# Optimization experiments

Measured on AMD Instinct MI355X. Metric: run time of the kernel, lower is better.

The kernel has to match this reference:

```python
import jax, jax.numpy as jnp
import numpy as np

B, N, D, CI, CO = 16, 1024, 16, 128, 128
ITERS = 3
EPS_BN = 1e-5
EPS_SQ = 1e-8


def sparsemax(z, axis):
    # Martins & Astudillo sparsemax along `axis`.
    K = z.shape[axis]
    z_s = jnp.flip(jnp.sort(z, axis=axis), axis=axis)  # descending
    z_cum = jnp.cumsum(z_s, axis=axis)
    shp = [1] * z.ndim
    shp[axis] = K
    k = jnp.arange(1, K + 1, dtype=z.dtype).reshape(shp)
    support = 1.0 + k * z_s > z_cum
    k_z = jnp.sum(support, axis=axis, keepdims=True).astype(z.dtype)
    tau_sum = jnp.sum(jnp.where(support, z_s, 0.0), axis=axis, keepdims=True)
    tau = (tau_sum - 1.0) / k_z
    return jnp.maximum(z - tau, 0.0)


def squash(s, axis):
    sq = jnp.sum(s * s, axis=axis, keepdims=True)
    return (sq / (1.0 + sq)) * s / jnp.sqrt(sq + EPS_SQ)


def setup_inputs() -> dict:
    key = jax.random.key(0)
    ks = jax.random.split(key, 4)
    x = jax.random.normal(ks[0], (B, N, CI), jnp.float32)
    a = jax.random.uniform(ks[1], (B, N, N), jnp.float32)
    adj = (a < 0.02).astype(jnp.float32)
    adj = jnp.maximum(adj, jnp.swapaxes(adj, -1, -2))  # symmetric 0/1 adjacency
    bn_gamma = jnp.ones((CI,), jnp.float32)
    bn_beta = jnp.zeros((CI,), jnp.float32)
    W = jax.random.normal(ks[2], (D, CI, CO), jnp.float32) / np.sqrt(CI)
    bias = jnp.zeros((D, CO), jnp.float32)
    return {"x": x, "adj": adj, "bn_gamma": bn_gamma, "bn_beta": bn_beta,
            "W": W, "bias": bias}


def _forward(x, adj, bn_gamma, bn_beta, W, bias):
    # BatchNorm1d, training-mode batch stats over flattened [B*N, CI]
    xf = x.reshape(-1, x.shape[-1])
    mu = xf.mean(0)
    var = ((xf - mu) ** 2).mean(0)  # biased variance (torch BN normalization)
    xn = (x - mu) / jnp.sqrt(var + EPS_BN) * bn_gamma + bn_beta

    # DenseGCNConv per digit capsule; adjacency normalization is shared.
    n = adj.shape[-1]
    eye = jnp.eye(n, dtype=adj.dtype)
    a = adj * (1.0 - eye) + eye                    # diag set to 1 (self-loops)
    dis = jnp.clip(a.sum(-1), 1.0, None) ** -0.5
    a_norm = dis[:, :, None] * a * dis[:, None, :]  # D^-1/2 A D^-1/2
    xw = jnp.einsum('bni,dio->bndo', xn, W)
    u = jnp.einsum('bmn,bndo->bmdo', a_norm, xw) + bias  # u_hat [B,N,D,CO]

    u_det = jax.lax.stop_gradient(u)  # torch uses u_hat.detach() in the loop
    b = jnp.zeros(u.shape[:3], u.dtype)  # [B,N,D]
    for _ in range(ITERS - 1):
        c = sparsemax(b, axis=2)
        s = jnp.einsum('bnd,bndo->bdo', c, u_det)
        v = squash(s, axis=-1)  # squash over capsule dim (dim=-2 in torch view)
        b = b + jnp.einsum('bndo,bdo->bnd', u_det, v)

    c = sparsemax(b, axis=2)
    s = jnp.einsum('bnd,bndo->bdo', c, u)
    s = s + xn.mean(1)[:, None, :]  # residual; broadcasts over D (needs CI==CO)
    # Original squashes with dim=-1 over a trailing singleton -> elementwise squash
    sq = s * s
    v = (sq / (1.0 + sq)) * s / jnp.sqrt(sq + EPS_SQ)

    adj_out = jnp.einsum('bnd,bnm,bme->bde', c, adj, c)  # coarsened adjacency
    return v, adj_out


def reference(x, adj, bn_gamma, bn_beta, W, bias):
    return _forward(x, adj, bn_gamma, bn_beta, W, bias)
```

## Files before the change

kernel.cpp:

```cpp
#include <hip/hip_runtime.h>

#define NB 16
#define NN 1024
#define ND 16
#define NCI 128
#define NCO 128
#define BN_ROWS (NB*NN)
#define MAXDEG 128
#define VOFF_ADJ (NB*ND*NCO)

__device__ __forceinline__ void fma4(float4& a, float s, const float4& w) {
    a.x = fmaf(s, w.x, a.x); a.y = fmaf(s, w.y, a.y);
    a.z = fmaf(s, w.z, a.z); a.w = fmaf(s, w.w, a.w);
}
__device__ __forceinline__ void add4(float4& a, const float4& b) {
    a.x += b.x; a.y += b.y; a.z += b.z; a.w += b.w;
}

__global__ __launch_bounds__(256) void k_pre1(const float* __restrict__ x,
                                              float* __restrict__ pbn,
                                              const float* __restrict__ W,
                                              float* __restrict__ Wt) {
    __shared__ float4 ls[8][32], lq[8][32];
    __shared__ float tile[32][33];
    int t = threadIdx.x;
    if (blockIdx.x < 256) {
        int q = t & 31, rg = t >> 5;
        int row0 = blockIdx.x * 64;
        const float4* x4 = (const float4*)x;
        float4 s = make_float4(0, 0, 0, 0), sq = make_float4(0, 0, 0, 0);
        for (int r = rg; r < 64; r += 8) {
            float4 v = x4[(size_t)(row0 + r) * 32 + q];
            s.x += v.x; s.y += v.y; s.z += v.z; s.w += v.w;
            sq.x = fmaf(v.x, v.x, sq.x); sq.y = fmaf(v.y, v.y, sq.y);
            sq.z = fmaf(v.z, v.z, sq.z); sq.w = fmaf(v.w, v.w, sq.w);
        }
        ls[rg][q] = s; lq[rg][q] = sq;
        __syncthreads();
        if (t < 32) {
            float4 a = ls[0][t];
            #pragma unroll
            for (int r = 1; r < 8; ++r) add4(a, ls[r][t]);
            ((float4*)(pbn + (size_t)blockIdx.x * 256))[t] = a;
        } else if (t < 64) {
            int qq = t - 32;
            float4 a = lq[0][qq];
            #pragma unroll
            for (int r = 1; r < 8; ++r) add4(a, lq[r][qq]);
            ((float4*)(pbn + (size_t)blockIdx.x * 256 + 128))[qq] = a;
        }
    } else {
        int d = blockIdx.x - 256;
        int r = t >> 5, cq = t & 31;
        const float* Wd = W + (size_t)d * NCI * NCO;
        float* Wtd = Wt + (size_t)d * NCI * NCO;
        for (int ti = 0; ti < 4; ++ti)
            for (int tj = 0; tj < 4; ++tj) {
                __syncthreads();
                for (int rr = r; rr < 32; rr += 8)
                    tile[rr][cq] = Wd[(size_t)(ti * 32 + rr) * 128 + tj * 32 + cq];
                __syncthreads();
                for (int rr = r; rr < 32; rr += 8)
                    Wtd[(size_t)(tj * 32 + rr) * 128 + ti * 32 + cq] = tile[cq][rr];
            }
    }
}

__global__ __launch_bounds__(256) void k_pre2(const float* __restrict__ adj,
        float* __restrict__ dis, int* __restrict__ nbr_idx, int* __restrict__ nbr_cnt,
        float* __restrict__ selfd, const float* __restrict__ pbn,
        const float* __restrict__ gamma, const float* __restrict__ beta,
        float* __restrict__ ss, float* __restrict__ xm) {
    int t = threadIdx.x;
    if (blockIdx.x < NB * NN) {
        int bm = blockIdx.x;
        int m = bm & (NN - 1);
        const float4* row4 = (const float4*)(adj + (size_t)bm * NN);
        __shared__ int cnt;
        __shared__ int idx[MAXDEG];
        if (t == 0) { cnt = 1; idx[0] = m; }
        __syncthreads();
        float4 v = row4[t];
        int n0 = t * 4;
        float av[4] = {v.x, v.y, v.z, v.w};
        #pragma unroll
        for (int j = 0; j < 4; ++j) {
            int n = n0 + j;
            if (n == m) {
                selfd[bm] = (av[j] > 0.5f) ? 1.f : 0.f;
            } else if (av[j] > 0.5f) {
                int p = atomicAdd(&cnt, 1);
                if (p < MAXDEG) idx[p] = n;
            }
        }
        __syncthreads();
        int c = min(cnt, MAXDEG);
        if (t == 0) {
            nbr_cnt[bm] = c;
            dis[bm] = rsqrtf((float)c);
        }
        for (int k = t; k < c; k += 256) nbr_idx[(size_t)bm * MAXDEG + k] = idx[k];
    } else {
        int b = blockIdx.x - NB * NN;
        if (t < 128) {
            float s = 0.f, sq = 0.f, sb = 0.f;
            for (int blk = 0; blk < 256; ++blk) {
                float v = pbn[(size_t)blk * 256 + t];
                s += v;
                sq += pbn[(size_t)blk * 256 + 128 + t];
                sb += ((blk >> 4) == b) ? v : 0.f;
            }
            float mu = s * (1.f / BN_ROWS);
            float var = sq * (1.f / BN_ROWS) - mu * mu;
            float sc = gamma[t] * rsqrtf(var + 1e-5f);
            float sh = beta[t] - mu * sc;
            if (b == 0) { ss[t] = sc; ss[128 + t] = sh; }
            xm[b * NCI + t] = sb * (1.f / NN) * sc + sh;
        }
    }
}

__global__ void k_y(const float* __restrict__ x, const float* __restrict__ ss,
                    const float* __restrict__ dis, const int* __restrict__ nbr_idx,
                    const int* __restrict__ nbr_cnt, float* __restrict__ y) {
    int l = blockIdx.x;
    int idx0 = l >> 3;
    int b = (l & 7) + ((idx0 >> 10) << 3);
    int m = idx0 & 1023;
    int bm = (b << 10) + m;
    int t = threadIdx.x;
    int q = t & 31, ng = t >> 5;
    __shared__ float sw[MAXDEG];
    __shared__ int sIdx[MAXDEG];
    int cnt = nbr_cnt[bm];
    float dm = dis[bm];
    for (int k = t; k < cnt; k += 128) {
        int n = nbr_idx[(size_t)bm * MAXDEG + k];
        sIdx[k] = n;
        sw[k] = dm * dis[(b << 10) + n];
    }
    __syncthreads();
    const float4* xb = (const float4*)(x + ((size_t)(b << 10)) * NCI);
    float4 acc = make_float4(0, 0, 0, 0);
    float wsum = 0.f;
    for (int k = ng; k < cnt; k += 4) {
        float w = sw[k];
        float4 v = xb[(size_t)sIdx[k] * 32 + q];
        fma4(acc, w, v);
        wsum += w;
    }
    __shared__ float4 lacc[4][32];
    __shared__ float lws[4];
    lacc[ng][q] = acc;
    if (q == 0) lws[ng] = wsum;
    __syncthreads();
    if (t < 32) {
        float4 a = lacc[0][t];
        add4(a, lacc[1][t]); add4(a, lacc[2][t]); add4(a, lacc[3][t]);
        float wst = lws[0] + lws[1] + lws[2] + lws[3];
        float4 sc = ((const float4*)ss)[t];
        float4 sh = ((const float4*)(ss + 128))[t];
        float4 o;
        o.x = sc.x * a.x + sh.x * wst;
        o.y = sc.y * a.y + sh.y * wst;
        o.z = sc.z * a.z + sh.z * wst;
        o.w = sc.w * a.w + sh.w * wst;
        ((float4*)(y + (size_t)bm * NCI))[t] = o;
    }
}

__device__ __forceinline__ void sv_phase(int b, int d, int t, int mode,
    const float* __restrict__ gsrc, const float* __restrict__ pcs,
    const float* __restrict__ W, const float* __restrict__ Wt,
    const float* __restrict__ bias, const float* __restrict__ xm,
    float* __restrict__ hbuf, float* __restrict__ hbb, float* __restrict__ outv,
    float* gl, float4 (*red)[32], float* redf, float* svec, float* vvv,
    float* csum_s, float* scal)
{
    if (mode == 0) {
        int q = t & 31, rg = t >> 5;
        const float4* yb = (const float4*)(gsrc + (((size_t)b) << 10) * NCI);
        float4 s = make_float4(0, 0, 0, 0);
        #pragma unroll 4
        for (int r = rg; r < 1024; r += 8) add4(s, yb[(size_t)r * 32 + q]);
        red[rg][q] = s;
        if (t == 0) *csum_s = 64.f;
        __syncthreads();
        if (t < 32) {
            float4 a = red[0][t];
            #pragma unroll
            for (int r = 1; r < 8; ++r) add4(a, red[r][t]);
            a.x *= (1.f / 16.f); a.y *= (1.f / 16.f);
            a.z *= (1.f / 16.f); a.w *= (1.f / 16.f);
            ((float4*)gl)[t] = a;
        }
        __syncthreads();
    } else {
        int col = t & 127, half = t >> 7;
        float g = 0.f;
        #pragma unroll 4
        for (int ch = half * 16; ch < half * 16 + 16; ++ch)
            g += gsrc[(((size_t)b * 32 + ch) * 16 + d) * NCI + col];
        ((float*)red)[half * 128 + col] = g;
        if (t == 0) {
            float cs = 0.f;
            #pragma unroll
            for (int ch = 0; ch < 32; ++ch) cs += pcs[(b * 32 + ch) * 16 + d];
            *csum_s = cs;
        }
        __syncthreads();
        if (t < 128) gl[t] = ((float*)red)[t] + ((float*)red)[128 + t];
        __syncthreads();
    }

    {
        int q = t & 31, hh = t >> 5;
        const float4* Wd4 = (const float4*)(W + (size_t)d * NCI * NCO);
        float4 acc = make_float4(0, 0, 0, 0);
        for (int i = hh * 16; i < hh * 16 + 16; ++i)
            fma4(acc, gl[i], Wd4[(size_t)i * 32 + q]);
        red[hh][q] = acc;
    }
    __syncthreads();
    if (t < 32) {
        float4 a = red[0][t];
        #pragma unroll
        for (int r = 1; r < 8; ++r) add4(a, red[r][t]);
        float4 b4 = ((const float4*)(bias + d * NCO))[t];
        float cs = *csum_s;
        a.x = fmaf(cs, b4.x, a.x); a.y = fmaf(cs, b4.y, a.y);
        a.z = fmaf(cs, b4.z, a.z); a.w = fmaf(cs, b4.w, a.w);
        ((float4*)svec)[t] = a;
    }
    __syncthreads();

    if (mode == 2) {
        if (t < 128) {
            float sv2 = svec[t] + xm[b * NCO + t];
            float sq = sv2 * sv2;
            outv[(size_t)(b * 16 + d) * NCO + t] = (sq / (1.f + sq)) * sv2 * rsqrtf(sq + 1e-8f);
        }
        return;
    }

    redf[t] = (t < 128) ? svec[t] * svec[t] : 0.f;
    __syncthreads();
    if (t < 64) {
        float val = redf[t] + redf[t + 64] + redf[t + 128] + redf[t + 192];
        #pragma unroll
        for (int m2 = 32; m2 >= 1; m2 >>= 1) val += __shfl_xor(val, m2);
        if (t == 0) *scal = val;
    }
    __syncthreads();
    if (t < 128) {
        float tot = *scal;
        vvv[t] = (tot / (1.f + tot)) * svec[t] * rsqrtf(tot + 1e-8f);
    }
    __syncthreads();

    {
        int q = t & 31, hh = t >> 5;
        const float4* Wt4 = (const float4*)(Wt + (size_t)d * NCI * NCO);
        float4 acc = make_float4(0, 0, 0, 0);
        for (int o = hh * 16; o < hh * 16 + 16; ++o)
            fma4(acc, vvv[o], Wt4[(size_t)o * 32 + q]);
        red[hh][q] = acc;
    }
    redf[t] = (t < 128) ? bias[d * NCO + t] * vvv[t] : 0.f;
    __syncthreads();
    if (t < 32) {
        float4 a = red[0][t];
        #pragma unroll
        for (int r = 1; r < 8; ++r) add4(a, red[r][t]);
        ((float4*)(hbuf + (size_t)(b * 16 + d) * NCI))[t] = a;
    }
    if (t >= 64 && t < 128) {
        int tt = t - 64;
        float val = redf[tt] + redf[tt + 64] + redf[tt + 128] + redf[tt + 192];
        #pragma unroll
        for (int m2 = 32; m2 >= 1; m2 >>= 1) val += __shfl_xor(val, m2);
        if (tt == 0) hbb[b * 16 + d] = val;
    }
}

__global__ __launch_bounds__(256) void k_sv(const float* __restrict__ gsrc,
        const float* __restrict__ pcs, const float* __restrict__ W,
        const float* __restrict__ Wt, const float* __restrict__ bias,
        const float* __restrict__ xm, float* __restrict__ hbuf,
        float* __restrict__ hbb, float* __restrict__ outv, int mode) {
    __shared__ float gl[128], svec[128], vvv[128];
    __shared__ float4 red[8][32];
    __shared__ float redf[256];
    __shared__ float csum_s, scal;
    int l = blockIdx.x, idx0 = l >> 3;
    int b = (l & 7) + ((idx0 >> 4) << 3);
    int d = idx0 & 15;
    sv_phase(b, d, threadIdx.x, mode, gsrc, pcs, W, Wt, bias, xm,
             hbuf, hbb, outv, gl, red, redf, svec, vvv, &csum_s, &scal);
}

__global__ __launch_bounds__(256) void k_bgc(const float* __restrict__ y,
        const float* __restrict__ hbuf, const float* __restrict__ hbb,
        float* __restrict__ blog, float* __restrict__ cglob,
        float* __restrict__ pg, float* __restrict__ pcs,
        float* __restrict__ outz, int first, int last) {
    int l = blockIdx.x, idx0 = l >> 3;
    int b = (l & 7) + ((idx0 >> 5) << 3);
    int j = idx0 & 31;
    int t = threadIdx.x;
    int n0 = j * 32;
    __shared__ __align__(16) float sy[32 * 128];
    __shared__ __align__(16) float sh[16 * 132];
    __shared__ float shb[16];
    __shared__ float scd[32][17];
    {
        const float4* hb4 = (const float4*)(hbuf + (size_t)b * 16 * NCI);
        float4* sh4 = (float4*)sh;
        for (int jj = t; jj < 16 * 32; jj += 256) {
            int row = jj >> 5, col = jj & 31;
            sh4[row * 33 + col] = hb4[row * 32 + col];
        }
        const float4* yb4 = (const float4*)(y + (((size_t)b << 10) + n0) * NCI);
        float4* sy4 = (float4*)sy;
        for (int jj = t; jj < 32 * 32; jj += 256) sy4[jj] = yb4[jj];
        if (t < 16) shb[t] = hbb[b * 16 + t];
    }
    __syncthreads();
    int nsub = t >> 4, d = t & 15;
    #pragma unroll
    for (int nn = nsub; nn < 32; nn += 16) {
        float acc = 0.f;
        const float* yr = &sy[nn * 128];
        const float* hr = &sh[d * 132];
        #pragma unroll 8
        for (int i = 0; i < 128; i += 4) {
            float4 a = *(const float4*)&yr[i];
            float4 h4 = *(const float4*)&hr[i];
            acc = fmaf(a.x, h4.x, acc);
            acc = fmaf(a.y, h4.y, acc);
            acc = fmaf(a.z, h4.z, acc);
            acc = fmaf(a.w, h4.w, acc);
        }
        size_t idx = (((size_t)b << 10) + n0 + nn) * ND + d;
        float bnew = acc + shb[d] + (first ? 0.f : blog[idx]);
        if (!last) blog[idx] = bnew;
        scd[nn][d] = bnew;
    }
    __syncthreads();
    if (t < 32) {
        float z[16], zs[16];
        #pragma unroll
        for (int d2 = 0; d2 < 16; ++d2) { z[d2] = scd[t][d2]; zs[d2] = z[d2]; }
        #pragma unroll
        for (int a = 0; a < 16; ++a) {
            #pragma unroll
            for (int b2 = a + 1; b2 < 16; ++b2) {
                float hi = fmaxf(zs[a], zs[b2]);
                float lo = fminf(zs[a], zs[b2]);
                zs[a] = hi; zs[b2] = lo;
            }
        }
        float cs = 0.f, tausum = 0.f;
        int kz = 1;
        #pragma unroll
        for (int k = 1; k <= 16; ++k) {
            cs += zs[k - 1];
            if (1.f + (float)k * zs[k - 1] > cs) { kz = k; tausum = cs; }
        }
        float tau = (tausum - 1.f) / (float)kz;
        #pragma unroll
        for (int d2 = 0; d2 < 16; ++d2) scd[t][d2] = fmaxf(z[d2] - tau, 0.f);
    }
    __syncthreads();
    if (last) {
        for (int jj = t; jj < 32 * 16; jj += 256)
            cglob[(((size_t)b << 10) + n0 + (jj >> 4)) * ND + (jj & 15)] = scd[jj >> 4][jj & 15];
        if (j == 0) outz[VOFF_ADJ + b * 256 + t] = 0.f;
    }
    if (t < 16) {
        float cs = 0.f;
        #pragma unroll 4
        for (int nn = 0; nn < 32; ++nn) cs += scd[nn][t];
        pcs[(b * 32 + j) * 16 + t] = cs;
    }
    int col = t & 127, dh = t >> 7;
    float accg[8] = {};
    for (int nn = 0; nn < 32; ++nn) {
        float yv = sy[nn * 128 + col];
        #pragma unroll
        for (int dd = 0; dd < 8; ++dd) accg[dd] = fmaf(scd[nn][dh * 8 + dd], yv, accg[dd]);
    }
    #pragma unroll
    for (int dd = 0; dd < 8; ++dd)
        pg[(((size_t)b * 32 + j) * 16 + dh * 8 + dd) * NCI + col] = accg[dd];
}

__global__ __launch_bounds__(256) void k_svt(const float* __restrict__ pg,
        const float* __restrict__ pcs, const float* __restrict__ W,
        const float* __restrict__ Wt, const float* __restrict__ bias,
        const float* __restrict__ xm, float* __restrict__ hbuf,
        float* __restrict__ hbb, const float* __restrict__ cglob,
        const int* __restrict__ nbr_idx, const int* __restrict__ nbr_cnt,
        const float* __restrict__ selfd, float* __restrict__ outv) {
    __shared__ float gl[128], svec[128], vvv[128];
    __shared__ float4 red[8][32];
    __shared__ float redf[256];
    __shared__ float csum_s, scal;
    __shared__ float cm[32][17], tm[32][17];
    int t = threadIdx.x;
    if (blockIdx.x < 256) {
        int l = blockIdx.x, idx0 = l >> 3;
        int b = (l & 7) + ((idx0 >> 4) << 3);
        int d = idx0 & 15;
        sv_phase(b, d, t, 2, pg, pcs, W, Wt, bias, xm,
                 hbuf, hbb, outv, gl, red, redf, svec, vvv, &csum_s, &scal);
        return;
    }
    int l2 = blockIdx.x - 256, idx0 = l2 >> 3;
    int b = (l2 & 7) + ((idx0 >> 5) << 3);
    int j = idx0 & 31;
    for (int jj = t; jj < 32 * 16; jj += 256)
        cm[jj >> 4][jj & 15] = cglob[(((size_t)b << 10) + j * 32 + (jj >> 4)) * ND + (jj & 15)];
    __syncthreads();
    int w = t >> 6, tg = t & 63, nsub = tg >> 4, d = tg & 15;
    for (int mm = w; mm < 32; mm += 4) {
        int m = j * 32 + mm;
        int bm = (b << 10) + m;
        int cnt = nbr_cnt[bm];
        float acc = 0.f;
        for (int k = nsub; k < cnt; k += 4) {
            int n = nbr_idx[(size_t)bm * MAXDEG + k];
            acc += cglob[(((size_t)b << 10) + n) * ND + d];
        }
        acc += __shfl_xor(acc, 16);
        acc += __shfl_xor(acc, 32);
        if (tg < 16) {
            if (selfd[bm] == 0.f) acc -= cm[mm][d];
            tm[mm][d] = acc;
        }
    }
    __syncthreads();
    int d2 = t >> 4, e2 = t & 15;
    float s = 0.f;
    #pragma unroll 8
    for (int mm = 0; mm < 32; ++mm) s = fmaf(tm[mm][d2], cm[mm][e2], s);
    atomicAdd(&outv[VOFF_ADJ + b * 256 + t], s);
}

extern "C" void kernel_launch(void* const* d_in, const int* in_sizes, int n_in,
                              void* d_out, int out_size, void* d_ws, size_t ws_size,
                              hipStream_t stream) {
    const float* x     = (const float*)d_in[0];
    const float* adj   = (const float*)d_in[1];
    const float* gamma = (const float*)d_in[2];
    const float* beta  = (const float*)d_in[3];
    const float* W     = (const float*)d_in[4];
    const float* bias  = (const float*)d_in[5];
    float* out = (float*)d_out;

    char* wptr = (char*)d_ws;
    size_t used = 0;
    auto alloc = [&](size_t nbytes) -> void* {
        void* p = wptr + used;
        used += (nbytes + 255) & ~(size_t)255;
        return p;
    };
    float* pbn     = (float*)alloc((size_t)256 * 256 * 4);
    float* ss      = (float*)alloc(256 * 4);
    float* xm      = (float*)alloc((size_t)NB * NCI * 4);
    float* dis     = (float*)alloc((size_t)NB * NN * 4);
    float* selfd   = (float*)alloc((size_t)NB * NN * 4);
    int*   nbr_cnt = (int*)alloc((size_t)NB * NN * 4);
    float* Wt      = (float*)alloc((size_t)ND * NCI * NCO * 4);
    float* y       = (float*)alloc((size_t)NB * NN * NCI * 4);
    float* blog    = (float*)alloc((size_t)NB * NN * ND * 4);
    float* cglob   = (float*)alloc((size_t)NB * NN * ND * 4);
    float* pg      = (float*)alloc((size_t)NB * 32 * ND * NCI * 4);
    float* pcs     = (float*)alloc((size_t)NB * 32 * ND * 4);
    float* hbuf    = (float*)alloc((size_t)NB * ND * NCI * 4);
    float* hbb     = (float*)alloc((size_t)NB * ND * 4);
    int*   nbr_idx = (int*)alloc((size_t)NB * NN * MAXDEG * 4);
    if (used > ws_size) return;

    k_pre1<<<256 + ND, 256, 0, stream>>>(x, pbn, W, Wt);
    k_pre2<<<NB * NN + NB, 256, 0, stream>>>(adj, dis, nbr_idx, nbr_cnt, selfd,
                                             pbn, gamma, beta, ss, xm);
    k_y<<<NB * NN, 128, 0, stream>>>(x, ss, dis, nbr_idx, nbr_cnt, y);

    k_sv<<<NB * ND, 256, 0, stream>>>(y, pcs, W, Wt, bias, xm, hbuf, hbb, out, 0);
    k_bgc<<<NB * 32, 256, 0, stream>>>(y, hbuf, hbb, blog, cglob, pg, pcs, out, 1, 0);
    k_sv<<<NB * ND, 256, 0, stream>>>(pg, pcs, W, Wt, bias, xm, hbuf, hbb, out, 1);
    k_bgc<<<NB * 32, 256, 0, stream>>>(y, hbuf, hbb, blog, cglob, pg, pcs, out, 0, 1);
    k_svt<<<256 + NB * 32, 256, 0, stream>>>(pg, pcs, W, Wt, bias, xm, hbuf, hbb,
                                             cglob, nbr_idx, nbr_cnt, selfd, out);
}
```

Measured before the change: 138.2 us.

## Fuse sv and bgc routing kernels with per-batch atomic flag handoff

```diff
diff --git a/kernel.cpp b/kernel.cpp
--- a/kernel.cpp
+++ b/kernel.cpp
@@ -122,13 +122,15 @@
 
 __global__ void k_y(const float* __restrict__ x, const float* __restrict__ ss,
                     const float* __restrict__ dis, const int* __restrict__ nbr_idx,
-                    const int* __restrict__ nbr_cnt, float* __restrict__ y) {
+                    const int* __restrict__ nbr_cnt, float* __restrict__ y,
+                    int* __restrict__ done) {
     int l = blockIdx.x;
     int idx0 = l >> 3;
     int b = (l & 7) + ((idx0 >> 10) << 3);
     int m = idx0 & 1023;
     int bm = (b << 10) + m;
     int t = threadIdx.x;
+    if (l == 0 && t < 32) done[t] = 0;
     int q = t & 31, ng = t >> 5;
     __shared__ float sw[MAXDEG];
     __shared__ int sIdx[MAXDEG];
@@ -283,36 +285,61 @@
     }
 }
 
-__global__ __launch_bounds__(256) void k_sv(const float* __restrict__ gsrc,
-        const float* __restrict__ pcs, const float* __restrict__ W,
-        const float* __restrict__ Wt, const float* __restrict__ bias,
-        const float* __restrict__ xm, float* __restrict__ hbuf,
-        float* __restrict__ hbb, float* __restrict__ outv, int mode) {
-    __shared__ float gl[128], svec[128], vvv[128];
-    __shared__ float4 red[8][32];
-    __shared__ float redf[256];
-    __shared__ float csum_s, scal;
-    int l = blockIdx.x, idx0 = l >> 3;
-    int b = (l & 7) + ((idx0 >> 4) << 3);
-    int d = idx0 & 15;
-    sv_phase(b, d, threadIdx.x, mode, gsrc, pcs, W, Wt, bias, xm,
-             hbuf, hbb, outv, gl, red, redf, svec, vvv, &csum_s, &scal);
-}
-
-__global__ __launch_bounds__(256) void k_bgc(const float* __restrict__ y,
-        const float* __restrict__ hbuf, const float* __restrict__ hbb,
+__global__ __launch_bounds__(256) void k_f(const float* __restrict__ y,
+        const float* __restrict__ W, const float* __restrict__ Wt,
+        const float* __restrict__ bias, const float* __restrict__ xm,
+        float* __restrict__ hbuf, float* __restrict__ hbb,
         float* __restrict__ blog, float* __restrict__ cglob,
         float* __restrict__ pg, float* __restrict__ pcs,
-        float* __restrict__ outz, int first, int last) {
-    int l = blockIdx.x, idx0 = l >> 3;
-    int b = (l & 7) + ((idx0 >> 5) << 3);
+        float* __restrict__ outv, int* __restrict__ done, int iter) {
+    __shared__ __align__(16) char smem[27136];
+    int t = threadIdx.x;
+    int* flag = done + (iter == 2 ? 16 : 0);
+
+    if (blockIdx.x < 256) {
+        float* gl   = (float*)(smem);
+        float* svec = (float*)(smem + 512);
+        float* vvv  = (float*)(smem + 1024);
+        float4 (*red)[32] = (float4 (*)[32])(smem + 1536);
+        float* redf = (float*)(smem + 5632);
+        float* csum_s = (float*)(smem + 6656);
+        float* scal   = (float*)(smem + 6660);
+        int l = blockIdx.x, idx0 = l >> 3;
+        int b = (l & 7) + ((idx0 >> 4) << 3);
+        int d = idx0 & 15;
+        sv_phase(b, d, t, (iter == 1) ? 0 : 1, (iter == 1) ? y : pg, pcs,
+                 W, Wt, bias, xm, hbuf, hbb, outv,
+                 gl, red, redf, svec, vvv, csum_s, scal);
+        __syncthreads();
+        if (t == 0) {
+            __threadfence();
+            __hip_atomic_fetch_add(&flag[b], 1, __ATOMIC_RELEASE, __HIP_MEMORY_SCOPE_AGENT);
+        }
+        return;
+    }
+
+    float* sy  = (float*)(smem);
+    float* sh  = (float*)(smem + 16384);
+    float* shb = (float*)(smem + 24832);
+    float (*scd)[17] = (float (*)[17])(smem + 24896);
+    int l2 = blockIdx.x - 256, idx0 = l2 >> 3;
+    int b = (l2 & 7) + ((idx0 >> 5) << 3);
     int j = idx0 & 31;
-    int t = threadIdx.x;
     int n0 = j * 32;
-    __shared__ __align__(16) float sy[32 * 128];
-    __shared__ __align__(16) float sh[16 * 132];
-    __shared__ float shb[16];
-    __shared__ float scd[32][17];
+    int first = (iter == 1), last = (iter == 2);
+
+    {
+        const float4* yb4 = (const float4*)(y + (((size_t)b << 10) + n0) * NCI);
+        float4* sy4 = (float4*)sy;
+        for (int jj = t; jj < 32 * 32; jj += 256) sy4[jj] = yb4[jj];
+    }
+    __syncthreads();
+    if (t == 0) {
+        while (__hip_atomic_load(&flag[b], __ATOMIC_ACQUIRE, __HIP_MEMORY_SCOPE_AGENT) < 16)
+            __builtin_amdgcn_s_sleep(8);
+        __threadfence();
+    }
+    __syncthreads();
     {
         const float4* hb4 = (const float4*)(hbuf + (size_t)b * 16 * NCI);
         float4* sh4 = (float4*)sh;
@@ -320,9 +347,6 @@
             int row = jj >> 5, col = jj & 31;
             sh4[row * 33 + col] = hb4[row * 32 + col];
         }
-        const float4* yb4 = (const float4*)(y + (((size_t)b << 10) + n0) * NCI);
-        float4* sy4 = (float4*)sy;
-        for (int jj = t; jj < 32 * 32; jj += 256) sy4[jj] = yb4[jj];
         if (t < 16) shb[t] = hbb[b * 16 + t];
     }
     __syncthreads();
@@ -375,7 +399,7 @@
     if (last) {
         for (int jj = t; jj < 32 * 16; jj += 256)
             cglob[(((size_t)b << 10) + n0 + (jj >> 4)) * ND + (jj & 15)] = scd[jj >> 4][jj & 15];
-        if (j == 0) outz[VOFF_ADJ + b * 256 + t] = 0.f;
+        if (j == 0) outv[VOFF_ADJ + b * 256 + t] = 0.f;
     }
     if (t < 16) {
         float cs = 0.f;
@@ -466,6 +490,7 @@
         return p;
     };
     float* pbn     = (float*)alloc((size_t)256 * 256 * 4);
+    int*   done    = (int*)alloc(32 * 4);
     float* ss      = (float*)alloc(256 * 4);
     float* xm      = (float*)alloc((size_t)NB * NCI * 4);
     float* dis     = (float*)alloc((size_t)NB * NN * 4);
@@ -485,12 +510,12 @@
     k_pre1<<<256 + ND, 256, 0, stream>>>(x, pbn, W, Wt);
     k_pre2<<<NB * NN + NB, 256, 0, stream>>>(adj, dis, nbr_idx, nbr_cnt, selfd,
                                              pbn, gamma, beta, ss, xm);
-    k_y<<<NB * NN, 128, 0, stream>>>(x, ss, dis, nbr_idx, nbr_cnt, y);
-
-    k_sv<<<NB * ND, 256, 0, stream>>>(y, pcs, W, Wt, bias, xm, hbuf, hbb, out, 0);
-    k_bgc<<<NB * 32, 256, 0, stream>>>(y, hbuf, hbb, blog, cglob, pg, pcs, out, 1, 0);
-    k_sv<<<NB * ND, 256, 0, stream>>>(pg, pcs, W, Wt, bias, xm, hbuf, hbb, out, 1);
-    k_bgc<<<NB * 32, 256, 0, stream>>>(y, hbuf, hbb, blog, cglob, pg, pcs, out, 0, 1);
+    k_y<<<NB * NN, 128, 0, stream>>>(x, ss, dis, nbr_idx, nbr_cnt, y, done);
+
+    k_f<<<768, 256, 0, stream>>>(y, W, Wt, bias, xm, hbuf, hbb, blog, cglob,
+                                 pg, pcs, out, done, 1);
+    k_f<<<768, 256, 0, stream>>>(y, W, Wt, bias, xm, hbuf, hbb, blog, cglob,
+                                 pg, pcs, out, done, 2);
     k_svt<<<256 + NB * 32, 256, 0, stream>>>(pg, pcs, W, Wt, bias, xm, hbuf, hbb,
                                              cglob, nbr_idx, nbr_cnt, selfd, out);
 }
```

After: 358.4 us. +159.4%, slower.

## Fuse all routing iterations into one persistent per-batch kernel

Applied to the files above, without the earlier changes.

```diff
diff --git a/kernel.cpp b/kernel.cpp
--- a/kernel.cpp
+++ b/kernel.cpp
@@ -169,255 +169,197 @@
     }
 }
 
-__device__ __forceinline__ void sv_phase(int b, int d, int t, int mode,
-    const float* __restrict__ gsrc, const float* __restrict__ pcs,
-    const float* __restrict__ W, const float* __restrict__ Wt,
-    const float* __restrict__ bias, const float* __restrict__ xm,
-    float* __restrict__ hbuf, float* __restrict__ hbb, float* __restrict__ outv,
-    float* gl, float4 (*red)[32], float* redf, float* svec, float* vvv,
-    float* csum_s, float* scal)
-{
-    if (mode == 0) {
+__global__ __launch_bounds__(1024) void k_route(const float* __restrict__ y,
+        const float* __restrict__ W, const float* __restrict__ Wt,
+        const float* __restrict__ bias, const float* __restrict__ xm,
+        float* __restrict__ blog, float* __restrict__ cglob,
+        float* __restrict__ outv) {
+    int b = blockIdx.x;
+    int t = threadIdx.x;
+    int wv = t >> 6;
+    int ln = t & 63;
+
+    __shared__ float sy[32 * 132];
+    __shared__ float hb[16][132];
+    __shared__ float gb[16][129];
+    __shared__ float svv[16][132];
+    __shared__ float scd[32][17];
+    __shared__ float csum[16], hbbs[16];
+
+    const float4* yb4 = (const float4*)(y + (((size_t)b) << 10) * NCI);
+
+    {
         int q = t & 31, rg = t >> 5;
-        const float4* yb = (const float4*)(gsrc + (((size_t)b) << 10) * NCI);
         float4 s = make_float4(0, 0, 0, 0);
-        #pragma unroll 4
-        for (int r = rg; r < 1024; r += 8) add4(s, yb[(size_t)r * 32 + q]);
-        red[rg][q] = s;
-        if (t == 0) *csum_s = 64.f;
+        for (int r = rg; r < 1024; r += 32) add4(s, yb4[(size_t)r * 32 + q]);
+        ((float4*)sy)[rg * 32 + q] = s;
+        if (t < 16) csum[t] = 64.f;
         __syncthreads();
         if (t < 32) {
-            float4 a = red[0][t];
-            #pragma unroll
-            for (int r = 1; r < 8; ++r) add4(a, red[r][t]);
+            float4 a = ((float4*)sy)[t];
+            for (int r = 1; r < 32; ++r) add4(a, ((float4*)sy)[r * 32 + t]);
             a.x *= (1.f / 16.f); a.y *= (1.f / 16.f);
             a.z *= (1.f / 16.f); a.w *= (1.f / 16.f);
-            ((float4*)gl)[t] = a;
-        }
-        __syncthreads();
-    } else {
-        int col = t & 127, half = t >> 7;
-        float g = 0.f;
-        #pragma unroll 4
-        for (int ch = half * 16; ch < half * 16 + 16; ++ch)
-            g += gsrc[(((size_t)b * 32 + ch) * 16 + d) * NCI + col];
-        ((float*)red)[half * 128 + col] = g;
-        if (t == 0) {
-            float cs = 0.f;
-            #pragma unroll
-            for (int ch = 0; ch < 32; ++ch) cs += pcs[(b * 32 + ch) * 16 + d];
-            *csum_s = cs;
-        }
-        __syncthreads();
-        if (t < 128) gl[t] = ((float*)red)[t] + ((float*)red)[128 + t];
-        __syncthreads();
-    }
-
-    {
-        int q = t & 31, hh = t >> 5;
-        const float4* Wd4 = (const float4*)(W + (size_t)d * NCI * NCO);
-        float4 acc = make_float4(0, 0, 0, 0);
-        for (int i = hh * 16; i < hh * 16 + 16; ++i)
-            fma4(acc, gl[i], Wd4[(size_t)i * 32 + q]);
-        red[hh][q] = acc;
-    }
-    __syncthreads();
-    if (t < 32) {
-        float4 a = red[0][t];
-        #pragma unroll
-        for (int r = 1; r < 8; ++r) add4(a, red[r][t]);
-        float4 b4 = ((const float4*)(bias + d * NCO))[t];
-        float cs = *csum_s;
-        a.x = fmaf(cs, b4.x, a.x); a.y = fmaf(cs, b4.y, a.y);
-        a.z = fmaf(cs, b4.z, a.z); a.w = fmaf(cs, b4.w, a.w);
-        ((float4*)svec)[t] = a;
-    }
-    __syncthreads();
-
-    if (mode == 2) {
-        if (t < 128) {
-            float sv2 = svec[t] + xm[b * NCO + t];
-            float sq = sv2 * sv2;
-            outv[(size_t)(b * 16 + d) * NCO + t] = (sq / (1.f + sq)) * sv2 * rsqrtf(sq + 1e-8f);
-        }
-        return;
-    }
-
-    redf[t] = (t < 128) ? svec[t] * svec[t] : 0.f;
-    __syncthreads();
-    if (t < 64) {
-        float val = redf[t] + redf[t + 64] + redf[t + 128] + redf[t + 192];
-        #pragma unroll
-        for (int m2 = 32; m2 >= 1; m2 >>= 1) val += __shfl_xor(val, m2);
-        if (t == 0) *scal = val;
-    }
-    __syncthreads();
-    if (t < 128) {
-        float tot = *scal;
-        vvv[t] = (tot / (1.f + tot)) * svec[t] * rsqrtf(tot + 1e-8f);
-    }
-    __syncthreads();
-
-    {
-        int q = t & 31, hh = t >> 5;
-        const float4* Wt4 = (const float4*)(Wt + (size_t)d * NCI * NCO);
-        float4 acc = make_float4(0, 0, 0, 0);
-        for (int o = hh * 16; o < hh * 16 + 16; ++o)
-            fma4(acc, vvv[o], Wt4[(size_t)o * 32 + q]);
-        red[hh][q] = acc;
-    }
-    redf[t] = (t < 128) ? bias[d * NCO + t] * vvv[t] : 0.f;
-    __syncthreads();
-    if (t < 32) {
-        float4 a = red[0][t];
-        #pragma unroll
-        for (int r = 1; r < 8; ++r) add4(a, red[r][t]);
-        ((float4*)(hbuf + (size_t)(b * 16 + d) * NCI))[t] = a;
-    }
-    if (t >= 64 && t < 128) {
-        int tt = t - 64;
-        float val = redf[tt] + redf[tt + 64] + redf[tt + 128] + redf[tt + 192];
-        #pragma unroll
-        for (int m2 = 32; m2 >= 1; m2 >>= 1) val += __shfl_xor(val, m2);
-        if (tt == 0) hbb[b * 16 + d] = val;
-    }
-}
-
-__global__ __launch_bounds__(256) void k_sv(const float* __restrict__ gsrc,
-        const float* __restrict__ pcs, const float* __restrict__ W,
-        const float* __restrict__ Wt, const float* __restrict__ bias,
-        const float* __restrict__ xm, float* __restrict__ hbuf,
-        float* __restrict__ hbb, float* __restrict__ outv, int mode) {
-    __shared__ float gl[128], svec[128], vvv[128];
-    __shared__ float4 red[8][32];
-    __shared__ float redf[256];
-    __shared__ float csum_s, scal;
-    int l = blockIdx.x, idx0 = l >> 3;
-    int b = (l & 7) + ((idx0 >> 4) << 3);
-    int d = idx0 & 15;
-    sv_phase(b, d, threadIdx.x, mode, gsrc, pcs, W, Wt, bias, xm,
-             hbuf, hbb, outv, gl, red, redf, svec, vvv, &csum_s, &scal);
-}
-
-__global__ __launch_bounds__(256) void k_bgc(const float* __restrict__ y,
-        const float* __restrict__ hbuf, const float* __restrict__ hbb,
-        float* __restrict__ blog, float* __restrict__ cglob,
-        float* __restrict__ pg, float* __restrict__ pcs,
-        float* __restrict__ outz, int first, int last) {
+            ((float4*)&gb[0][0])[t] = a;
+        }
+        __syncthreads();
+    }
+
+    for (int iter = 0; iter < 3; ++iter) {
+        int guni = (iter == 0);
+        int final_it = (iter == 2);
+        int d = wv;
+        {
+            const float* grow = gb[guni ? 0 : d];
+            const float2* W2 = (const float2*)(W + (size_t)d * NCI * NCO);
+            const float2* B2 = (const float2*)(bias + d * NCO);
+            float2 acc = make_float2(0.f, 0.f);
+            #pragma unroll 4
+            for (int i = 0; i < 128; ++i) {
+                float gv = grow[i];
+                float2 w2 = W2[i * 64 + ln];
+                acc.x = fmaf(gv, w2.x, acc.x);
+                acc.y = fmaf(gv, w2.y, acc.y);
+            }
+            float cs = csum[d];
+            float2 b2 = B2[ln];
+            acc.x = fmaf(cs, b2.x, acc.x);
+            acc.y = fmaf(cs, b2.y, acc.y);
+            if (final_it) {
+                int o0 = ln * 2;
+                float s0 = acc.x + xm[b * NCO + o0];
+                float s1 = acc.y + xm[b * NCO + o0 + 1];
+                float q0 = s0 * s0, q1 = s1 * s1;
+                outv[(size_t)(b * 16 + d) * NCO + o0]     = (q0 / (1.f + q0)) * s0 * rsqrtf(q0 + 1e-8f);
+                outv[(size_t)(b * 16 + d) * NCO + o0 + 1] = (q1 / (1.f + q1)) * s1 * rsqrtf(q1 + 1e-8f);
+            } else {
+                float val = acc.x * acc.x + acc.y * acc.y;
+                #pragma unroll
+                for (int m2 = 32; m2 >= 1; m2 >>= 1) val += __shfl_xor(val, m2);
+                float fac = (val / (1.f + val)) * rsqrtf(val + 1e-8f);
+                float v0 = fac * acc.x, v1 = fac * acc.y;
+                svv[d][ln * 2] = v0; svv[d][ln * 2 + 1] = v1;
+                float pb = b2.x * v0 + b2.y * v1;
+                #pragma unroll
+                for (int m2 = 32; m2 >= 1; m2 >>= 1) pb += __shfl_xor(pb, m2);
+                if (ln == 0) hbbs[d] = pb;
+            }
+        }
+        if (final_it) break;
+        __syncthreads();
+        {
+            const float2* Wt2 = (const float2*)(Wt + (size_t)d * NCI * NCO);
+            float2 acc = make_float2(0.f, 0.f);
+            #pragma unroll 4
+            for (int o = 0; o < 128; ++o) {
+                float vv = svv[d][o];
+                float2 w2 = Wt2[o * 64 + ln];
+                acc.x = fmaf(vv, w2.x, acc.x);
+                acc.y = fmaf(vv, w2.y, acc.y);
+            }
+            hb[d][ln * 2] = acc.x; hb[d][ln * 2 + 1] = acc.y;
+        }
+        __syncthreads();
+        {
+            int j = t * 2;
+            gb[j >> 7][j & 127] = 0.f;
+            gb[(j + 1) >> 7][(j + 1) & 127] = 0.f;
+            if (t < 16) csum[t] = 0.f;
+        }
+        __syncthreads();
+        for (int ch = 0; ch < 32; ++ch) {
+            int n0 = ch * 32;
+            {
+                int row = t >> 5, col = t & 31;
+                ((float4*)&sy[row * 132])[col] = yb4[(size_t)(n0 + row) * 32 + col];
+            }
+            __syncthreads();
+            {
+                int half = t & 1, task = t >> 1;
+                int nn = task >> 4, dd = task & 15;
+                const float* yr = &sy[nn * 132];
+                const float* hr = &hb[dd][0];
+                float acc = 0.f;
+                int i0 = half * 64;
+                #pragma unroll 4
+                for (int i = i0; i < i0 + 64; i += 4) {
+                    float4 a = *(const float4*)&yr[i];
+                    float4 h4 = *(const float4*)&hr[i];
+                    acc = fmaf(a.x, h4.x, acc);
+                    acc = fmaf(a.y, h4.y, acc);
+                    acc = fmaf(a.z, h4.z, acc);
+                    acc = fmaf(a.w, h4.w, acc);
+                }
+                acc += __shfl_xor(acc, 1);
+                if (half == 0) {
+                    size_t gidx = (((size_t)b << 10) + n0 + nn) * ND + dd;
+                    float bnew = acc + hbbs[dd] + (iter == 0 ? 0.f : blog[gidx]);
+                    if (iter == 0) blog[gidx] = bnew;
+                    scd[nn][dd] = bnew;
+                }
+            }
+            __syncthreads();
+            if (t < 32) {
+                float z[16], zs[16];
+                #pragma unroll
+                for (int d2 = 0; d2 < 16; ++d2) { z[d2] = scd[t][d2]; zs[d2] = z[d2]; }
+                #pragma unroll
+                for (int a = 0; a < 16; ++a) {
+                    #pragma unroll
+                    for (int b2 = a + 1; b2 < 16; ++b2) {
+                        float hi = fmaxf(zs[a], zs[b2]);
+                        float lo = fminf(zs[a], zs[b2]);
+                        zs[a] = hi; zs[b2] = lo;
+                    }
+                }
+                float cs = 0.f, tausum = 0.f;
+                int kz = 1;
+                #pragma unroll
+                for (int k = 1; k <= 16; ++k) {
+                    cs += zs[k - 1];
+                    if (1.f + (float)k * zs[k - 1] > cs) { kz = k; tausum = cs; }
+                }
+                float tau = (tausum - 1.f) / (float)kz;
+                #pragma unroll
+                for (int d2 = 0; d2 < 16; ++d2) {
+                    float cv = fmaxf(z[d2] - tau, 0.f);
+                    scd[t][d2] = cv;
+                    if (iter == 1)
+                        cglob[(((size_t)b << 10) + n0 + t) * ND + d2] = cv;
+                }
+            }
+            __syncthreads();
+            {
+                int i = t & 127, grp = t >> 7;
+                int d0 = grp * 2;
+                float a0 = 0.f, a1 = 0.f;
+                for (int nn = 0; nn < 32; ++nn) {
+                    float yv = sy[nn * 132 + i];
+                    a0 = fmaf(scd[nn][d0], yv, a0);
+                    a1 = fmaf(scd[nn][d0 + 1], yv, a1);
+                }
+                gb[d0][i] += a0;
+                gb[d0 + 1][i] += a1;
+            }
+            if (t < 16) {
+                float cs = 0.f;
+                #pragma unroll 4
+                for (int nn = 0; nn < 32; ++nn) cs += scd[nn][t];
+                csum[t] += cs;
+            }
+            __syncthreads();
+        }
+    }
+    if (t < 256) outv[VOFF_ADJ + b * 256 + t] = 0.f;
+}
+
+__global__ __launch_bounds__(256) void k_adjc(const float* __restrict__ cglob,
+        const int* __restrict__ nbr_idx, const int* __restrict__ nbr_cnt,
+        const float* __restrict__ selfd, float* __restrict__ outv) {
+    __shared__ float cm[32][17], tm[32][17];
+    int t = threadIdx.x;
     int l = blockIdx.x, idx0 = l >> 3;
     int b = (l & 7) + ((idx0 >> 5) << 3);
-    int j = idx0 & 31;
-    int t = threadIdx.x;
-    int n0 = j * 32;
-    __shared__ __align__(16) float sy[32 * 128];
-    __shared__ __align__(16) float sh[16 * 132];
-    __shared__ float shb[16];
-    __shared__ float scd[32][17];
-    {
-        const float4* hb4 = (const float4*)(hbuf + (size_t)b * 16 * NCI);
-        float4* sh4 = (float4*)sh;
-        for (int jj = t; jj < 16 * 32; jj += 256) {
-            int row = jj >> 5, col = jj & 31;
-            sh4[row * 33 + col] = hb4[row * 32 + col];
-        }
-        const float4* yb4 = (const float4*)(y + (((size_t)b << 10) + n0) * NCI);
-        float4* sy4 = (float4*)sy;
-        for (int jj = t; jj < 32 * 32; jj += 256) sy4[jj] = yb4[jj];
-        if (t < 16) shb[t] = hbb[b * 16 + t];
-    }
-    __syncthreads();
-    int nsub = t >> 4, d = t & 15;
-    #pragma unroll
-    for (int nn = nsub; nn < 32; nn += 16) {
-        float acc = 0.f;
-        const float* yr = &sy[nn * 128];
-        const float* hr = &sh[d * 132];
-        #pragma unroll 8
-        for (int i = 0; i < 128; i += 4) {
-            float4 a = *(const float4*)&yr[i];
-            float4 h4 = *(const float4*)&hr[i];
-            acc = fmaf(a.x, h4.x, acc);
-            acc = fmaf(a.y, h4.y, acc);
-            acc = fmaf(a.z, h4.z, acc);
-            acc = fmaf(a.w, h4.w, acc);
-        }
-        size_t idx = (((size_t)b << 10) + n0 + nn) * ND + d;
-        float bnew = acc + shb[d] + (first ? 0.f : blog[idx]);
-        if (!last) blog[idx] = bnew;
-        scd[nn][d] = bnew;
-    }
-    __syncthreads();
-    if (t < 32) {
-        float z[16], zs[16];
-        #pragma unroll
-        for (int d2 = 0; d2 < 16; ++d2) { z[d2] = scd[t][d2]; zs[d2] = z[d2]; }
-        #pragma unroll
-        for (int a = 0; a < 16; ++a) {
-            #pragma unroll
-            for (int b2 = a + 1; b2 < 16; ++b2) {
-                float hi = fmaxf(zs[a], zs[b2]);
-                float lo = fminf(zs[a], zs[b2]);
-                zs[a] = hi; zs[b2] = lo;
-            }
-        }
-        float cs = 0.f, tausum = 0.f;
-        int kz = 1;
-        #pragma unroll
-        for (int k = 1; k <= 16; ++k) {
-            cs += zs[k - 1];
-            if (1.f + (float)k * zs[k - 1] > cs) { kz = k; tausum = cs; }
-        }
-        float tau = (tausum - 1.f) / (float)kz;
-        #pragma unroll
-        for (int d2 = 0; d2 < 16; ++d2) scd[t][d2] = fmaxf(z[d2] - tau, 0.f);
-    }
-    __syncthreads();
-    if (last) {
-        for (int jj = t; jj < 32 * 16; jj += 256)
-            cglob[(((size_t)b << 10) + n0 + (jj >> 4)) * ND + (jj & 15)] = scd[jj >> 4][jj & 15];
-        if (j == 0) outz[VOFF_ADJ + b * 256 + t] = 0.f;
-    }
-    if (t < 16) {
-        float cs = 0.f;
-        #pragma unroll 4
-        for (int nn = 0; nn < 32; ++nn) cs += scd[nn][t];
-        pcs[(b * 32 + j) * 16 + t] = cs;
-    }
-    int col = t & 127, dh = t >> 7;
-    float accg[8] = {};
-    for (int nn = 0; nn < 32; ++nn) {
-        float yv = sy[nn * 128 + col];
-        #pragma unroll
-        for (int dd = 0; dd < 8; ++dd) accg[dd] = fmaf(scd[nn][dh * 8 + dd], yv, accg[dd]);
-    }
-    #pragma unroll
-    for (int dd = 0; dd < 8; ++dd)
-        pg[(((size_t)b * 32 + j) * 16 + dh * 8 + dd) * NCI + col] = accg[dd];
-}
-
-__global__ __launch_bounds__(256) void k_svt(const float* __restrict__ pg,
-        const float* __restrict__ pcs, const float* __restrict__ W,
-        const float* __restrict__ Wt, const float* __restrict__ bias,
-        const float* __restrict__ xm, float* __restrict__ hbuf,
-        float* __restrict__ hbb, const float* __restrict__ cglob,
-        const int* __restrict__ nbr_idx, const int* __restrict__ nbr_cnt,
-        const float* __restrict__ selfd, float* __restrict__ outv) {
-    __shared__ float gl[128], svec[128], vvv[128];
-    __shared__ float4 red[8][32];
-    __shared__ float redf[256];
-    __shared__ float csum_s, scal;
-    __shared__ float cm[32][17], tm[32][17];
-    int t = threadIdx.x;
-    if (blockIdx.x < 256) {
-        int l = blockIdx.x, idx0 = l >> 3;
-        int b = (l & 7) + ((idx0 >> 4) << 3);
-        int d = idx0 & 15;
-        sv_phase(b, d, t, 2, pg, pcs, W, Wt, bias, xm,
-                 hbuf, hbb, outv, gl, red, redf, svec, vvv, &csum_s, &scal);
-        return;
-    }
-    int l2 = blockIdx.x - 256, idx0 = l2 >> 3;
-    int b = (l2 & 7) + ((idx0 >> 5) << 3);
     int j = idx0 & 31;
     for (int jj = t; jj < 32 * 16; jj += 256)
         cm[jj >> 4][jj & 15] = cglob[(((size_t)b << 10) + j * 32 + (jj >> 4)) * ND + (jj & 15)];
@@ -475,10 +417,6 @@
     float* y       = (float*)alloc((size_t)NB * NN * NCI * 4);
     float* blog    = (float*)alloc((size_t)NB * NN * ND * 4);
     float* cglob   = (float*)alloc((size_t)NB * NN * ND * 4);
-    float* pg      = (float*)alloc((size_t)NB * 32 * ND * NCI * 4);
-    float* pcs     = (float*)alloc((size_t)NB * 32 * ND * 4);
-    float* hbuf    = (float*)alloc((size_t)NB * ND * NCI * 4);
-    float* hbb     = (float*)alloc((size_t)NB * ND * 4);
     int*   nbr_idx = (int*)alloc((size_t)NB * NN * MAXDEG * 4);
     if (used > ws_size) return;
 
@@ -486,11 +424,6 @@
     k_pre2<<<NB * NN + NB, 256, 0, stream>>>(adj, dis, nbr_idx, nbr_cnt, selfd,
                                              pbn, gamma, beta, ss, xm);
     k_y<<<NB * NN, 128, 0, stream>>>(x, ss, dis, nbr_idx, nbr_cnt, y);
-
-    k_sv<<<NB * ND, 256, 0, stream>>>(y, pcs, W, Wt, bias, xm, hbuf, hbb, out, 0);
-    k_bgc<<<NB * 32, 256, 0, stream>>>(y, hbuf, hbb, blog, cglob, pg, pcs, out, 1, 0);
-    k_sv<<<NB * ND, 256, 0, stream>>>(pg, pcs, W, Wt, bias, xm, hbuf, hbb, out, 1);
-    k_bgc<<<NB * 32, 256, 0, stream>>>(y, hbuf, hbb, blog, cglob, pg, pcs, out, 0, 1);
-    k_svt<<<256 + NB * 32, 256, 0, stream>>>(pg, pcs, W, Wt, bias, xm, hbuf, hbb,
-                                             cglob, nbr_idx, nbr_cnt, selfd, out);
-}
+    k_route<<<NB, 1024, 0, stream>>>(y, W, Wt, bias, xm, blog, cglob, out);
+    k_adjc<<<NB * 32, 256, 0, stream>>>(cglob, nbr_idx, nbr_cnt, selfd, out);
+}
```

Result: slower. 502.2 us (+263.4%).
